# Performance work log

Measured on AMD Instinct MI355X. Metric: run time of the kernel, lower is better.

The kernel has to match this reference:

```python
import jax, jax.numpy as jnp
import numpy as np

K = 4          # neighbors
R = 2          # step_ratio
OUT = 64       # output_size

def knn_idx(x, k):
    # x: (B, C, N) -> indices of k nearest neighbors (incl. self): (B, N, k)
    xx = jnp.sum(x * x, axis=1)                       # (B, N)
    inner = jnp.einsum('bcn,bcm->bnm', x, x)          # (B, N, N)
    neg_dist = 2.0 * inner - xx[:, :, None] - xx[:, None, :]
    _, idx = jax.lax.top_k(neg_dist, k)               # largest neg_dist = nearest
    return idx

def setup_inputs() -> dict:
    key = jax.random.key(0)
    ks = jax.random.split(key, 7)
    B, C, N = 16, 64, 2048
    s = 0.05
    return {
        'x':  jax.random.normal(ks[0], (B, C, N), jnp.float32),
        'w1': jax.random.normal(ks[1], (OUT, 2 * C), jnp.float32) * s,
        'b1': jax.random.normal(ks[2], (OUT,), jnp.float32) * s,
        'w2': jax.random.normal(ks[3], (OUT * R, 2 * C + OUT), jnp.float32) * s,
        'b2': jax.random.normal(ks[4], (OUT * R,), jnp.float32) * s,
        'w3': jax.random.normal(ks[5], (OUT, OUT), jnp.float32) * s,
        'b3': jax.random.normal(ks[6], (OUT,), jnp.float32) * s,
    }

def reference(x, w1, b1, w2, b2, w3, b3):
    B, C, N = x.shape
    idx = knn_idx(x, K)                                # (B, N, K)
    xt = jnp.transpose(x, (0, 2, 1))                   # (B, N, C)
    neighbors = xt[jnp.arange(B)[:, None, None], idx]  # (B, N, K, C)
    center = jnp.broadcast_to(xt[:, :, None, :], neighbors.shape)
    feat = jnp.concatenate([center, neighbors], axis=-1)   # (B, N, K, 2C), minus_center=False
    # get_graph_feature returns (B, 2C, N, K); module permutes to (B, 2C, K, N)
    f = jnp.transpose(feat, (0, 3, 2, 1))              # (B, 2C, K, N)
    e1 = jnp.einsum('oc,bckn->bokn', w1, f) + b1[None, :, None, None]
    e = jax.nn.relu(jnp.concatenate([e1, f], axis=1))  # (B, 2C+OUT, K, N)
    e2 = jax.nn.relu(jnp.einsum('oc,bckn->bokn', w2, e) + b2[None, :, None, None])  # (B, OUT*R, K, N)
    # permute(0,2,3,1) -> (B,K,N,OUT*R), view -> (B,K,N*R,OUT), permute -> (B,OUT,K,N*R)
    e2 = jnp.transpose(e2, (0, 2, 3, 1)).reshape(B, K, N * R, OUT)
    e2 = jnp.transpose(e2, (0, 3, 1, 2))               # (B, OUT, K, N*R)
    e3 = jnp.einsum('oc,bckn->bokn', w3, e2) + b3[None, :, None, None]
    return jnp.max(e3, axis=2)                          # (B, OUT, N*R)
```

## Files before the change

kernel.cpp:

```cpp
#include <hip/hip_runtime.h>
#include <hip/hip_bf16.h>

#define BB 16
#define CC 64
#define NN 2048
#define KK 4
#define NPART 4
#define JPER (NN / NPART)
#define NCAND 32
#define RSTRIDE 80

typedef unsigned short u16;
typedef unsigned int u32;
typedef __attribute__((ext_vector_type(4))) float f32x4;
typedef __attribute__((ext_vector_type(16))) float f32x16;
typedef __attribute__((ext_vector_type(8))) short short8;

__device__ __forceinline__ float bf2f(u16 u) {
    unsigned int x = ((unsigned int)u) << 16;
    float f;
    __builtin_memcpy(&f, &x, 4);
    return f;
}
__device__ __forceinline__ u16 f2bf(float f) {
    __hip_bfloat16 h = __float2bfloat16(f);
    u16 u;
    __builtin_memcpy(&u, &h, 2);
    return u;
}
__device__ __forceinline__ unsigned int pk2(float a, float b) {
    return (unsigned int)f2bf(a) | ((unsigned int)f2bf(b) << 16);
}
__device__ __forceinline__ u32 umx(u32 a, u32 b) { return a > b ? a : b; }
__device__ __forceinline__ u32 umn(u32 a, u32 b) { return a < b ? a : b; }

__global__ __launch_bounds__(256) void k_prep(const float* __restrict__ x,
                                              float* __restrict__ xt,
                                              double* __restrict__ xx64,
                                              u16* __restrict__ xpk) {
    int b = blockIdx.y;
    int n = blockIdx.x * 256 + threadIdx.x;
    const float* xb = x + (size_t)b * CC * NN;
    float v[CC];
    float s = 0.f;
    double s64 = 0.0;
#pragma unroll
    for (int c = 0; c < CC; c++) {
        v[c] = xb[(size_t)c * NN + n];
        s = fmaf(v[c], v[c], s);
        s64 += (double)v[c] * (double)v[c];
    }
    float4* dst = (float4*)(xt + ((size_t)b * NN + n) * CC);
#pragma unroll
    for (int q = 0; q < 16; q++) {
        dst[q] = make_float4(v[4 * q], v[4 * q + 1], v[4 * q + 2], v[4 * q + 3]);
    }
    xx64[b * NN + n] = s64;
    u16* dp = xpk + ((size_t)b * NN + n) * RSTRIDE;
#pragma unroll
    for (int q = 0; q < 8; q++) {
        uint4 u;
        u.x = pk2(v[8 * q], v[8 * q + 1]);
        u.y = pk2(v[8 * q + 2], v[8 * q + 3]);
        u.z = pk2(v[8 * q + 4], v[8 * q + 5]);
        u.w = pk2(v[8 * q + 6], v[8 * q + 7]);
        *(uint4*)(dp + q * 8) = u;
    }
    u16 hi = f2bf(s);
    u16 lo = f2bf(s - bf2f(hi));
    uint4 u8;
    u8.x = (unsigned int)hi | ((unsigned int)lo << 16);
    u8.y = 0x00003F80u;
    u8.z = 0; u8.w = 0;
    *(uint4*)(dp + 64) = u8;
    uint4 z = {0, 0, 0, 0};
    *(uint4*)(dp + 72) = z;
}

__global__ __launch_bounds__(256) void k_wprep(const float* __restrict__ w1,
                                               const float* __restrict__ w2,
                                               const float* __restrict__ w3,
                                               u16* __restrict__ wb1,
                                               u16* __restrict__ wb2,
                                               u16* __restrict__ wb3) {
    int t = blockIdx.x * 256 + threadIdx.x;
    int stride = gridDim.x * 256;
    for (int idx = t; idx < 64 * 128; idx += stride) {
        int o = idx >> 7, k = idx & 127;
        int cb = o >> 4, lr = o & 15, ks = k >> 5, g = (k >> 3) & 3, e = k & 7;
        wb1[((cb * 4 + ks) * 64 + g * 16 + lr) * 8 + e] = f2bf(w1[idx]);
    }
    for (int idx = t; idx < 128 * 192; idx += stride) {
        int o = idx / 192, k = idx - o * 192;
        int cb = o >> 4, lr = o & 15, ks = k >> 5, g = (k >> 3) & 3, e = k & 7;
        wb2[((cb * 6 + ks) * 64 + g * 16 + lr) * 8 + e] = f2bf(w2[idx]);
    }
    for (int idx = t; idx < 64 * 64; idx += stride) {
        int o = idx >> 6, k = idx & 63;
        int cb = o >> 4, lr = o & 15, ks = k >> 5, g = (k >> 3) & 3, e = k & 7;
        wb3[((cb * 2 + ks) * 64 + g * 16 + lr) * 8 + e] = f2bf(w3[idx]);
    }
}

__global__ __launch_bounds__(256) void k_knn3(const u16* __restrict__ xpk,
                                              u16* __restrict__ cand) {
    int ib = blockIdx.x;
    int part = blockIdx.y;
    int b = blockIdx.z;
    int tid = threadIdx.x;
    int i0 = ib * 128;
    int j00 = part * JPER;

    __shared__ u16 Bb[2 * 2 * 10 * 32 * 8];

    int w = tid >> 6, l = tid & 63;
    int lc = l & 31, lh = l >> 5;
    int hb4 = lh * 4;

    short8 ifrag[5];
    {
        const u16* ip = xpk + ((size_t)b * NN + i0 + w * 32 + lc) * RSTRIDE + lh * 8;
#pragma unroll
        for (int ks = 0; ks < 4; ks++) ifrag[ks] = *(const short8*)(ip + ks * 16);
        short8 f4 = {0, 0, 0, 0, 0, 0, 0, 0};
        if (lh == 0) {
            f4[0] = (short)0xBF00;
            f4[1] = (short)0xBF00;
            f4[2] = (short)0x4300;
        }
        ifrag[4] = f4;
    }

    u32 v0 = 0, v1 = 0, v2 = 0, v3 = 0;

#define CE(a, b) { u32 mx_ = umx(a, b); b = umn(a, b); a = mx_; }

#define STAGE(rr, bf)                                                              \
    {                                                                              \
        int jb = j00 + (rr) * 64;                                                  \
        for (int g = tid; g < 640; g += 256) {                                     \
            int rw = g / 10, c = g - rw * 10;                                      \
            uint4 u = *(const uint4*)(xpk + ((size_t)b * NN + jb + rw) * RSTRIDE + \
                                      c * 8);                                      \
            int sub = rw >> 5, r32 = rw & 31;                                      \
            *(uint4*)((char*)Bb + (bf) * 10240 + sub * 5120 + c * 512 +            \
                      ((r32 ^ (c & 7)) * 16)) = u;                                 \
        }                                                                          \
    }

    STAGE(0, 0);

    for (int r = 0; r < JPER / 64; r++) {
        __syncthreads();
        if (r + 1 < JPER / 64) STAGE(r + 1, (r + 1) & 1);

        const char* bufp = (const char*)Bb + (r & 1) * 10240;
        f32x16 acc0, acc1;
#pragma unroll
        for (int e = 0; e < 16; e++) {
            acc0[e] = 0.f;
            acc1[e] = 0.f;
        }
#pragma unroll
        for (int ks = 0; ks < 5; ks++) {
            int c = ks * 2 + lh;
            int boff = c * 512 + ((lc ^ (c & 7)) * 16);
            short8 a0 = *(const short8*)(bufp + boff);
            short8 a1 = *(const short8*)(bufp + 5120 + boff);
            acc0 = __builtin_amdgcn_mfma_f32_32x32x16_bf16(a0, ifrag[ks], acc0, 0, 0, 0);
            acc1 = __builtin_amdgcn_mfma_f32_32x32x16_bf16(a1, ifrag[ks], acc1, 0, 0, 0);
        }
#pragma unroll
        for (int sub = 0; sub < 2; sub++) {
            const f32x16& acc = sub ? acc1 : acc0;
            int jlb = r * 64 + sub * 32 + hb4;
            u32 kk[16];
#pragma unroll
            for (int rg = 0; rg < 16; rg++) {
                u32 u;
                float f = acc[rg];
                __builtin_memcpy(&u, &f, 4);
                int coff = (rg & 3) + 8 * (rg >> 2);
                kk[rg] = (u & ~0x1FFu) | (u32)(jlb + coff);
            }
#pragma unroll
            for (int q = 0; q < 4; q++) {
                int p = q * 4;
                CE(kk[p + 0], kk[p + 2]); CE(kk[p + 1], kk[p + 3]);
                CE(kk[p + 0], kk[p + 1]); CE(kk[p + 2], kk[p + 3]);
                CE(kk[p + 1], kk[p + 2]);
            }
            kk[0] = umx(kk[0], kk[7]); kk[1] = umx(kk[1], kk[6]);
            kk[2] = umx(kk[2], kk[5]); kk[3] = umx(kk[3], kk[4]);
            CE(kk[0], kk[2]); CE(kk[1], kk[3]); CE(kk[0], kk[1]); CE(kk[2], kk[3]);
            kk[8] = umx(kk[8], kk[15]); kk[9] = umx(kk[9], kk[14]);
            kk[10] = umx(kk[10], kk[13]); kk[11] = umx(kk[11], kk[12]);
            CE(kk[8], kk[10]); CE(kk[9], kk[11]); CE(kk[8], kk[9]); CE(kk[10], kk[11]);
            kk[0] = umx(kk[0], kk[11]); kk[1] = umx(kk[1], kk[10]);
            kk[2] = umx(kk[2], kk[9]); kk[3] = umx(kk[3], kk[8]);
            CE(kk[0], kk[2]); CE(kk[1], kk[3]); CE(kk[0], kk[1]); CE(kk[2], kk[3]);
            v0 = umx(v0, kk[3]); v1 = umx(v1, kk[2]);
            v2 = umx(v2, kk[1]); v3 = umx(v3, kk[0]);
            CE(v0, v2); CE(v1, v3); CE(v0, v1); CE(v2, v3);
        }
    }
#undef STAGE
#undef CE

    size_t cb = ((size_t)b * NN + i0 + w * 32 + lc) * NCAND + part * 8 + lh * 4;
    cand[cb + 0] = (u16)(j00 + (v0 & 0x1FF));
    cand[cb + 1] = (u16)(j00 + (v1 & 0x1FF));
    cand[cb + 2] = (u16)(j00 + (v2 & 0x1FF));
    cand[cb + 3] = (u16)(j00 + (v3 & 0x1FF));
}

__global__ __launch_bounds__(256) void k_knn_merge(const float* __restrict__ xt,
                                                   const double* __restrict__ xx64,
                                                   const u16* __restrict__ cand,
                                                   int* __restrict__ nidx) {
    __shared__ double sv[16 * 33];
    __shared__ u16 ji[16 * 33];

    int tid = threadIdx.x;
    int g = tid >> 4;
    int q = tid & 15;
    size_t gp0 = (size_t)blockIdx.x * 16;
    size_t bbase = (gp0 >> 11) << 11;

    for (int idx = tid; idx < 16 * 32; idx += 256) {
        int p = idx >> 5, c = idx & 31;
        ji[p * 33 + c] = cand[(gp0 + p) * NCAND + c];
    }
    __syncthreads();

    float4 a = ((const float4*)(xt + (gp0 + g) * CC))[q];

#pragma unroll 4
    for (int c = 0; c < NCAND; c++) {
        int j = ji[g * 33 + c];
        float4 bv = ((const float4*)(xt + (bbase + j) * CC))[q];
        double d = (double)a.x * (double)bv.x + (double)a.y * (double)bv.y +
                   (double)a.z * (double)bv.z + (double)a.w * (double)bv.w;
        d += __shfl_xor(d, 8);
        d += __shfl_xor(d, 4);
        d += __shfl_xor(d, 2);
        d += __shfl_xor(d, 1);
        if (q == 0) sv[g * 33 + c] = 2.0 * d - xx64[bbase + j];
    }
    __syncthreads();

    if (tid < 16) {
        int p = tid;
        double v4[4];
        int id4[4];
#pragma unroll
        for (int s = 0; s < 4; s++) {
            v4[s] = -1e300;
            id4[s] = 0x7fffffff;
        }
        for (int cc = 0; cc < NCAND; cc++) {
            double cv = sv[p * 33 + cc];
            int ci = ji[p * 33 + cc];
#pragma unroll
            for (int s = 0; s < 4; s++) {
                bool take = (cv > v4[s]) || (cv == v4[s] && ci < id4[s]);
                double nv = take ? cv : v4[s];
                int ni = take ? ci : id4[s];
                double ov = take ? v4[s] : cv;
                int oi = take ? id4[s] : ci;
                v4[s] = nv;
                id4[s] = ni;
                cv = ov;
                ci = oi;
            }
        }
        size_t gp2 = gp0 + p;
#pragma unroll
        for (int s = 0; s < 4; s++) nidx[gp2 * 4 + s] = id4[s];
    }
}

__global__ __launch_bounds__(256) void k_mlp(const u16* __restrict__ xpk,
                                             const int* __restrict__ nidx,
                                             const u16* __restrict__ wb1,
                                             const u16* __restrict__ wb2,
                                             const u16* __restrict__ wb3,
                                             const float* __restrict__ b1,
                                             const float* __restrict__ b2,
                                             const float* __restrict__ b3,
                                             float* __restrict__ out) {
    int nch = blockIdx.x;
    int b = blockIdx.y;
    int n0 = nch * 16;
    int tid = threadIdx.x;

    __shared__ u16 Fb[64 * 128];
    __shared__ u16 E1b[64 * 64];
    __shared__ u16 E2b[64 * 128];
    __shared__ float Ob[64 * 36];
    __shared__ int ji[64];

    if (tid < 64) ji[tid] = nidx[((size_t)b * NN + n0) * KK + tid];
    __syncthreads();

    for (int g = tid; g < 64 * 16; g += 256) {
        int it = g >> 4, q = g & 15;
        int half = q >> 3, cq = q & 7;
        int srcn = half ? ji[it] : (n0 + (it >> 2));
        uint4 u = *(const uint4*)(xpk + ((size_t)b * NN + srcn) * RSTRIDE + cq * 8);
        int byte = (it * 256 + half * 128 + cq * 16) ^ ((it & 7) << 4);
        *(uint4*)((char*)Fb + byte) = u;
    }
    __syncthreads();

    int w = tid >> 6, l = tid & 63;
    int lr = l & 15, lg = l >> 4;

    {
        f32x4 acc[4];
#pragma unroll
        for (int g = 0; g < 4; g++) acc[g] = (f32x4){0.f, 0.f, 0.f, 0.f};
#pragma unroll
        for (int ks = 0; ks < 4; ks++) {
            short8 bw = *(const short8*)(wb1 + ((size_t)(w * 4 + ks) * 64 + l) * 8);
#pragma unroll
            for (int g = 0; g < 4; g++) {
                int arow = g * 16 + lr;
                int off = (arow * 256 + ks * 64 + lg * 16) ^ ((arow & 7) << 4);
                short8 a = *(const short8*)((const char*)Fb + off);
                acc[g] = __builtin_amdgcn_mfma_f32_16x16x32_bf16(a, bw, acc[g], 0, 0, 0);
            }
        }
        float bias = b1[w * 16 + lr];
#pragma unroll
        for (int g = 0; g < 4; g++) {
#pragma unroll
            for (int q = 0; q < 4; q++) {
                int item = g * 16 + lg * 4 + q;
                float vv = fmaxf(acc[g][q] + bias, 0.f);
                int byte = (item * 128 + (w * 16 + lr) * 2) ^ ((item & 7) << 4);
                *(u16*)((char*)E1b + byte) = f2bf(vv);
            }
        }
    }
    __syncthreads();

    {
        f32x4 acc[4][2];
#pragma unroll
        for (int g = 0; g < 4; g++)
#pragma unroll
            for (int c2 = 0; c2 < 2; c2++) acc[g][c2] = (f32x4){0.f, 0.f, 0.f, 0.f};
#pragma unroll
        for (int ks = 0; ks < 6; ks++) {
            short8 bw0 = *(const short8*)(wb2 + ((size_t)((w * 2) * 6 + ks) * 64 + l) * 8);
            short8 bw1 = *(const short8*)(wb2 + ((size_t)((w * 2 + 1) * 6 + ks) * 64 + l) * 8);
#pragma unroll
            for (int g = 0; g < 4; g++) {
                int arow = g * 16 + lr;
                int aswz = (arow & 7) << 4;
                short8 a;
                if (ks < 2) {
                    int off = (arow * 128 + ks * 64 + lg * 16) ^ aswz;
                    a = *(const short8*)((const char*)E1b + off);
                } else {
                    int off = (arow * 256 + (ks - 2) * 64 + lg * 16) ^ aswz;
                    uint4 u = *(const uint4*)((const char*)Fb + off);
                    unsigned int m;
                    m = ((u.x >> 15) & 0x10001u) * 0xFFFFu; u.x &= ~m;
                    m = ((u.y >> 15) & 0x10001u) * 0xFFFFu; u.y &= ~m;
                    m = ((u.z >> 15) & 0x10001u) * 0xFFFFu; u.z &= ~m;
                    m = ((u.w >> 15) & 0x10001u) * 0xFFFFu; u.w &= ~m;
                    __builtin_memcpy(&a, &u, 16);
                }
                acc[g][0] = __builtin_amdgcn_mfma_f32_16x16x32_bf16(a, bw0, acc[g][0], 0, 0, 0);
                acc[g][1] = __builtin_amdgcn_mfma_f32_16x16x32_bf16(a, bw1, acc[g][1], 0, 0, 0);
            }
        }
#pragma unroll
        for (int c2 = 0; c2 < 2; c2++) {
            float bias = b2[(w * 2 + c2) * 16 + lr];
#pragma unroll
            for (int g = 0; g < 4; g++) {
#pragma unroll
                for (int q = 0; q < 4; q++) {
                    int item = g * 16 + lg * 4 + q;
                    float vv = fmaxf(acc[g][c2][q] + bias, 0.f);
                    int byte = (item * 256 + ((w * 2 + c2) * 16 + lr) * 2) ^ ((item & 7) << 4);
                    *(u16*)((char*)E2b + byte) = f2bf(vv);
                }
            }
        }
    }
    __syncthreads();

    {
        f32x4 acc[4][2];
#pragma unroll
        for (int g = 0; g < 4; g++)
#pragma unroll
            for (int r = 0; r < 2; r++) acc[g][r] = (f32x4){0.f, 0.f, 0.f, 0.f};
#pragma unroll
        for (int ks = 0; ks < 2; ks++) {
            short8 bw = *(const short8*)(wb3 + ((size_t)(w * 2 + ks) * 64 + l) * 8);
#pragma unroll
            for (int g = 0; g < 4; g++) {
                int arow = g * 16 + lr;
                int aswz = (arow & 7) << 4;
#pragma unroll
                for (int r = 0; r < 2; r++) {
                    int off = (arow * 256 + r * 128 + ks * 64 + lg * 16) ^ aswz;
                    short8 a = *(const short8*)((const char*)E2b + off);
                    acc[g][r] = __builtin_amdgcn_mfma_f32_16x16x32_bf16(a, bw, acc[g][r], 0, 0, 0);
                }
            }
        }
        float bias = b3[w * 16 + lr];
        int o = w * 16 + lr;
#pragma unroll
        for (int g = 0; g < 4; g++) {
            int nl = g * 4 + lg;
#pragma unroll
            for (int r = 0; r < 2; r++) {
                float m = fmaxf(fmaxf(acc[g][r][0], acc[g][r][1]),
                                fmaxf(acc[g][r][2], acc[g][r][3])) + bias;
                Ob[o * 36 + nl * 2 + r] = m;
            }
        }
    }
    __syncthreads();

    {
        int o = tid >> 2, q = tid & 3;
        float4 v0 = *(const float4*)&Ob[o * 36 + q * 8];
        float4 v1 = *(const float4*)&Ob[o * 36 + q * 8 + 4];
        float* dst = out + ((size_t)(b * 64 + o)) * 4096 + n0 * 2 + q * 8;
        ((float4*)dst)[0] = v0;
        ((float4*)dst)[1] = v1;
    }
}

extern "C" void kernel_launch(void* const* d_in, const int* in_sizes, int n_in,
                              void* d_out, int out_size, void* d_ws, size_t ws_size,
                              hipStream_t stream) {
    const float* x = (const float*)d_in[0];
    const float* w1 = (const float*)d_in[1];
    const float* b1 = (const float*)d_in[2];
    const float* w2 = (const float*)d_in[3];
    const float* b2 = (const float*)d_in[4];
    const float* w3 = (const float*)d_in[5];
    const float* b3 = (const float*)d_in[6];
    float* out = (float*)d_out;

    float* xt = (float*)d_ws;
    u16* xpk = (u16*)(xt + (size_t)BB * NN * CC);
    double* xx64 = (double*)(xpk + (size_t)BB * NN * RSTRIDE);
    int* nidx = (int*)(xx64 + (size_t)BB * NN);
    u16* cand = (u16*)(nidx + (size_t)BB * NN * KK);
    u16* wb1 = cand + (size_t)BB * NN * NCAND;
    u16* wb2 = wb1 + 64 * 128;
    u16* wb3 = wb2 + 128 * 192;

    k_prep<<<dim3(NN / 256, BB), 256, 0, stream>>>(x, xt, xx64, xpk);
    k_wprep<<<dim3(32), 256, 0, stream>>>(w1, w2, w3, wb1, wb2, wb3);
    k_knn3<<<dim3(NN / 128, NPART, BB), 256, 0, stream>>>(xpk, cand);
    k_knn_merge<<<dim3(BB * NN / 16), 256, 0, stream>>>(xt, xx64, cand, nidx);
    k_mlp<<<dim3(NN / 16, BB), 256, 0, stream>>>(xpk, nidx, wb1, wb2, wb3, b1, b2, b3, out);
}
```

Baseline: 113.5 us.

## Parallelize kNN merge over candidates with four lanes per distance

Restructures the candidate rescoring kernel so each block handles 2 points instead of 16. Each group of 4 threads computes one candidate's fp64 distance over 16 channels, replacing the per-thread loop over 32 candidates with a 16-lane shuffle reduction. The grid grows by 8x, which gives more parallelism and shorter dependency chains per thread. In exchange it adds many more tiny blocks and a final top-4 selection step done by only 2 threads per block.

```diff
diff --git a/kernel.cpp b/kernel.cpp
--- a/kernel.cpp
+++ b/kernel.cpp
@@ -218,39 +218,42 @@
                                                    const double* __restrict__ xx64,
                                                    const u16* __restrict__ cand,
                                                    int* __restrict__ nidx) {
-    __shared__ double sv[16 * 33];
-    __shared__ u16 ji[16 * 33];
+    __shared__ double sv[2 * 33];
+    __shared__ int sj[2 * 33];
 
     int tid = threadIdx.x;
-    int g = tid >> 4;
-    int q = tid & 15;
-    size_t gp0 = (size_t)blockIdx.x * 16;
-    size_t bbase = (gp0 >> 11) << 11;
-
-    for (int idx = tid; idx < 16 * 32; idx += 256) {
-        int p = idx >> 5, c = idx & 31;
-        ji[p * 33 + c] = cand[(gp0 + p) * NCAND + c];
-    }
-    __syncthreads();
-
-    float4 a = ((const float4*)(xt + (gp0 + g) * CC))[q];
-
-#pragma unroll 4
-    for (int c = 0; c < NCAND; c++) {
-        int j = ji[g * 33 + c];
-        float4 bv = ((const float4*)(xt + (bbase + j) * CC))[q];
-        double d = (double)a.x * (double)bv.x + (double)a.y * (double)bv.y +
-                   (double)a.z * (double)bv.z + (double)a.w * (double)bv.w;
-        d += __shfl_xor(d, 8);
-        d += __shfl_xor(d, 4);
-        d += __shfl_xor(d, 2);
-        d += __shfl_xor(d, 1);
-        if (q == 0) sv[g * 33 + c] = 2.0 * d - xx64[bbase + j];
-    }
-    __syncthreads();
-
-    if (tid < 16) {
-        int p = tid;
+    int q = tid & 3;
+    int g = tid >> 2;
+    int p = g >> 5;
+    int c = g & 31;
+    size_t gp = (size_t)blockIdx.x * 2 + p;
+    size_t bbase = (gp >> 11) << 11;
+
+    int j = cand[gp * NCAND + c];
+    const float4* xi = (const float4*)(xt + gp * CC) + q * 4;
+    const float4* xj = (const float4*)(xt + (bbase + j) * CC) + q * 4;
+
+    float4 a0 = xi[0], a1 = xi[1], a2 = xi[2], a3 = xi[3];
+    float4 c0 = xj[0], c1 = xj[1], c2 = xj[2], c3 = xj[3];
+    double d0 = (double)a0.x * c0.x + (double)a0.y * c0.y +
+                (double)a0.z * c0.z + (double)a0.w * c0.w;
+    double d1 = (double)a1.x * c1.x + (double)a1.y * c1.y +
+                (double)a1.z * c1.z + (double)a1.w * c1.w;
+    double d2 = (double)a2.x * c2.x + (double)a2.y * c2.y +
+                (double)a2.z * c2.z + (double)a2.w * c2.w;
+    double d3 = (double)a3.x * c3.x + (double)a3.y * c3.y +
+                (double)a3.z * c3.z + (double)a3.w * c3.w;
+    double d = (d0 + d1) + (d2 + d3);
+    d += __shfl_xor(d, 1);
+    d += __shfl_xor(d, 2);
+    if (q == 0) {
+        sv[p * 33 + c] = 2.0 * d - xx64[bbase + j];
+        sj[p * 33 + c] = j;
+    }
+    __syncthreads();
+
+    if (tid < 2) {
+        int p2 = tid;
         double v4[4];
         int id4[4];
 #pragma unroll
@@ -259,8 +262,8 @@
             id4[s] = 0x7fffffff;
         }
         for (int cc = 0; cc < NCAND; cc++) {
-            double cv = sv[p * 33 + cc];
-            int ci = ji[p * 33 + cc];
+            double cv = sv[p2 * 33 + cc];
+            int ci = sj[p2 * 33 + cc];
 #pragma unroll
             for (int s = 0; s < 4; s++) {
                 bool take = (cv > v4[s]) || (cv == v4[s] && ci < id4[s]);
@@ -274,7 +277,7 @@
                 ci = oi;
             }
         }
-        size_t gp2 = gp0 + p;
+        size_t gp2 = (size_t)blockIdx.x * 2 + p2;
 #pragma unroll
         for (int s = 0; s < 4; s++) nidx[gp2 * 4 + s] = id4[s];
     }
@@ -464,6 +467,6 @@
     k_prep<<<dim3(NN / 256, BB), 256, 0, stream>>>(x, xt, xx64, xpk);
     k_wprep<<<dim3(32), 256, 0, stream>>>(w1, w2, w3, wb1, wb2, wb3);
     k_knn3<<<dim3(NN / 128, NPART, BB), 256, 0, stream>>>(xpk, cand);
-    k_knn_merge<<<dim3(BB * NN / 16), 256, 0, stream>>>(xt, xx64, cand, nidx);
+    k_knn_merge<<<dim3(BB * NN / 2), 256, 0, stream>>>(xt, xx64, cand, nidx);
     k_mlp<<<dim3(NN / 16, BB), 256, 0, stream>>>(xpk, nidx, wb1, wb2, wb3, b1, b2, b3, out);
 }
```

After: 133.1 us. +17.3%, slower.

## Restructure kNN merge to one wave per point with swizzled LDS row staging

Applied to the files above, without the earlier changes.

The kNN merge kernel now handles 4 points per block, one wavefront each, instead of 16 points with 16-lane groups. Each wave gathers its 32 candidate rows into LDS with an XOR swizzle, and lanes pair up to compute the fp64 dot products. That replaces the serialized per-candidate loop and its four-step shuffle reduction with parallel loads and a single shuffle. A block-index swizzle also changes the order in which points are visited. The cost is more blocks and about 35 KB of LDS per block, which may limit occupancy, and the top-4 selection still runs serially on a single lane.

```diff
diff --git a/kernel.cpp b/kernel.cpp
--- a/kernel.cpp
+++ b/kernel.cpp
@@ -218,39 +218,61 @@
                                                    const double* __restrict__ xx64,
                                                    const u16* __restrict__ cand,
                                                    int* __restrict__ nidx) {
-    __shared__ double sv[16 * 33];
-    __shared__ u16 ji[16 * 33];
+    __shared__ __align__(16) char rows[4 * 32 * 272];
+    __shared__ double svp[4 * 32];
+    __shared__ double sxx[4 * 32];
+    __shared__ u16 jc[4 * 32];
 
     int tid = threadIdx.x;
-    int g = tid >> 4;
-    int q = tid & 15;
-    size_t gp0 = (size_t)blockIdx.x * 16;
+    int w = tid >> 6;
+    int l = tid & 63;
+    int nwg8 = (int)(gridDim.x >> 3);
+    int swz = (blockIdx.x & 7) * nwg8 + (blockIdx.x >> 3);
+    size_t gp0 = (size_t)swz * 4;
     size_t bbase = (gp0 >> 11) << 11;
-
-    for (int idx = tid; idx < 16 * 32; idx += 256) {
-        int p = idx >> 5, c = idx & 31;
-        ji[p * 33 + c] = cand[(gp0 + p) * NCAND + c];
-    }
-    __syncthreads();
-
-    float4 a = ((const float4*)(xt + (gp0 + g) * CC))[q];
-
-#pragma unroll 4
-    for (int c = 0; c < NCAND; c++) {
-        int j = ji[g * 33 + c];
-        float4 bv = ((const float4*)(xt + (bbase + j) * CC))[q];
-        double d = (double)a.x * (double)bv.x + (double)a.y * (double)bv.y +
-                   (double)a.z * (double)bv.z + (double)a.w * (double)bv.w;
-        d += __shfl_xor(d, 8);
-        d += __shfl_xor(d, 4);
-        d += __shfl_xor(d, 2);
-        d += __shfl_xor(d, 1);
-        if (q == 0) sv[g * 33 + c] = 2.0 * d - xx64[bbase + j];
-    }
-    __syncthreads();
-
-    if (tid < 16) {
-        int p = tid;
+    size_t pt = gp0 + w;
+
+    if (l < 32) {
+        u16 j = cand[pt * NCAND + l];
+        jc[w * 32 + l] = j;
+        sxx[w * 32 + l] = xx64[bbase + j];
+    }
+    __syncthreads();
+
+    char* myrows = rows + w * 32 * 272;
+
+    {
+        int c = l & 15;
+        int r0 = l >> 4;
+#pragma unroll
+        for (int it = 0; it < 8; it++) {
+            int r = it * 4 + r0;
+            int j = jc[w * 32 + r];
+            float4 v = *(const float4*)(xt + (bbase + (size_t)j) * CC + c * 4);
+            int slot = c ^ ((r & 7) << 1);
+            *(float4*)(myrows + r * 272 + slot * 16) = v;
+        }
+    }
+
+    int k = l >> 1, h = l & 1;
+    const float4* ap = (const float4*)(xt + pt * CC + h * 32);
+    double d = 0.0;
+    {
+        const char* rb = myrows + k * 272;
+#pragma unroll
+        for (int i = 0; i < 8; i++) {
+            int cj = h * 8 + i;
+            int slot = cj ^ ((k & 7) << 1);
+            float4 bv = *(const float4*)(rb + slot * 16);
+            float4 av = ap[i];
+            d += (double)av.x * bv.x + (double)av.y * bv.y +
+                 (double)av.z * bv.z + (double)av.w * bv.w;
+        }
+    }
+    d += __shfl_xor(d, 1);
+    if (h == 0) svp[w * 32 + k] = 2.0 * d - sxx[w * 32 + k];
+
+    if (l == 0) {
         double v4[4];
         int id4[4];
 #pragma unroll
@@ -259,8 +281,8 @@
             id4[s] = 0x7fffffff;
         }
         for (int cc = 0; cc < NCAND; cc++) {
-            double cv = sv[p * 33 + cc];
-            int ci = ji[p * 33 + cc];
+            double cv = svp[w * 32 + cc];
+            int ci = jc[w * 32 + cc];
 #pragma unroll
             for (int s = 0; s < 4; s++) {
                 bool take = (cv > v4[s]) || (cv == v4[s] && ci < id4[s]);
@@ -274,9 +296,8 @@
                 ci = oi;
             }
         }
-        size_t gp2 = gp0 + p;
-#pragma unroll
-        for (int s = 0; s < 4; s++) nidx[gp2 * 4 + s] = id4[s];
+#pragma unroll
+        for (int s = 0; s < 4; s++) nidx[pt * 4 + s] = id4[s];
     }
 }
 
@@ -464,6 +485,6 @@
     k_prep<<<dim3(NN / 256, BB), 256, 0, stream>>>(x, xt, xx64, xpk);
     k_wprep<<<dim3(32), 256, 0, stream>>>(w1, w2, w3, wb1, wb2, wb3);
     k_knn3<<<dim3(NN / 128, NPART, BB), 256, 0, stream>>>(xpk, cand);
-    k_knn_merge<<<dim3(BB * NN / 16), 256, 0, stream>>>(xt, xx64, cand, nidx);
+    k_knn_merge<<<dim3(BB * NN / 4), 256, 0, stream>>>(xt, xx64, cand, nidx);
     k_mlp<<<dim3(NN / 16, BB), 256, 0, stream>>>(xpk, nidx, wb1, wb2, wb3, b1, b2, b3, out);
 }
```

Measured after the change: 166.0 us. 1.46x slower.
